# Kernel optimization log

Hardware: AMD Instinct MI355X
Metric: run time of the kernel (lower is better)

Reference implementation:

```python
import jax, jax.numpy as jnp
import numpy as np

D_PAIR = 128
N_HEAD = 4
D_HID = 32
SCALING = 1.0 / np.sqrt(D_HID)


def setup_inputs() -> dict:
    key = jax.random.key(0)
    ks = jax.random.split(key, 12)
    B, L = 1, 256
    s = 0.02
    return {
        "pair": jax.random.normal(ks[0], (B, L, L, D_PAIR), dtype=jnp.float32),
        "gamma": jnp.ones((D_PAIR,), jnp.float32),
        "beta": jnp.zeros((D_PAIR,), jnp.float32),
        "Wq": jax.random.normal(ks[1], (D_PAIR, N_HEAD * D_HID), jnp.float32) * s,
        "Wk": jax.random.normal(ks[2], (D_PAIR, N_HEAD * D_HID), jnp.float32) * s,
        "Wv": jax.random.normal(ks[3], (D_PAIR, N_HEAD * D_HID), jnp.float32) * s,
        "Wb": jax.random.normal(ks[4], (D_PAIR, N_HEAD), jnp.float32) * s,
        "Wg": jax.random.normal(ks[5], (D_PAIR, N_HEAD * D_HID), jnp.float32) * s,
        "bg": jnp.ones((N_HEAD * D_HID,), jnp.float32),
        "Wo": jax.random.normal(ks[6], (N_HEAD * D_HID, D_PAIR), jnp.float32) * s,
        "bo": jnp.zeros((D_PAIR,), jnp.float32),
    }


def _layernorm(x, gamma, beta, eps=1e-5):
    mu = jnp.mean(x, axis=-1, keepdims=True)
    var = jnp.var(x, axis=-1, keepdims=True)
    return (x - mu) * jax.lax.rsqrt(var + eps) * gamma + beta


def reference(pair, gamma, beta, Wq, Wk, Wv, Wb, Wg, bg, Wo, bo):
    B, L = pair.shape[:2]
    x = _layernorm(pair, gamma, beta)                      # (B,L,L,D)
    q = (x @ Wq).reshape(B, L, L, N_HEAD, D_HID) * SCALING  # (B,L,L,h,d)
    k = (x @ Wk).reshape(B, L, L, N_HEAD, D_HID)
    v = (x @ Wv).reshape(B, L, L, N_HEAD, D_HID)
    bias = x @ Wb                                           # (B,L,L,h)
    gate = jax.nn.sigmoid(x @ Wg + bg)                      # (B,L,L,h*d)
    # start_node=True: attend over ending index k of row i
    attn = jnp.einsum('bijhd,bikhd->bijkh', q, k)           # (B,L,L,L,h)
    attn = attn + bias[:, None]                             # bias[b,j,k,h] broadcast over i
    attn = jax.nn.softmax(attn, axis=-2)                    # over k
    out = jnp.einsum('bijkh,bikhd->bijhd', attn, v).reshape(B, L, L, N_HEAD * D_HID)
    out = gate * out
    return out @ Wo + bo
```

## Files before the change

kernel.cpp:

```cpp
#include <hip/hip_runtime.h>
#include <math.h>

#define L 256
#define DP 128
#define NH 4
#define DH 32
#define NROW 65536

typedef unsigned short ushort_t;
typedef __attribute__((ext_vector_type(8))) short short8;
typedef __attribute__((ext_vector_type(4))) float f32x4;
typedef __attribute__((ext_vector_type(4))) unsigned int u32x4;

constexpr float SCALING = 0.17677669529663687f;

static __device__ __forceinline__ unsigned short f2bf(float f) {
    unsigned u = __builtin_bit_cast(unsigned, f);
    u = u + 0x7fffu + ((u >> 16) & 1u);
    return (unsigned short)(u >> 16);
}
static __device__ __forceinline__ float bf2f(unsigned short h) {
    unsigned u = ((unsigned)h) << 16;
    return __builtin_bit_cast(float, u);
}
static __device__ __forceinline__ unsigned packbf(float lo, float hi) {
    return ((unsigned)f2bf(hi) << 16) | (unsigned)f2bf(lo);
}

__global__ __launch_bounds__(256) void prep_kernel(
    const float* __restrict__ Wq, const float* __restrict__ Wk, const float* __restrict__ Wv,
    const float* __restrict__ Wb, const float* __restrict__ Wg, const float* __restrict__ Wo,
    ushort_t* __restrict__ WtAll, ushort_t* __restrict__ WohT, ushort_t* __restrict__ WolT)
{
    int rowi = blockIdx.x * 16 + (threadIdx.x >> 4);
    int d0 = (threadIdx.x & 15) * 8;
    #pragma unroll
    for (int dd = 0; dd < 8; ++dd) {
        int d = d0 + dd;
        if (rowi < 512) {
            int n = rowi & 127;
            float val;
            if (rowi < 128)      val = Wq[d * 128 + n] * SCALING;
            else if (rowi < 256) val = Wk[d * 128 + n];
            else if (rowi < 384) val = Wv[d * 128 + n];
            else                 val = Wg[d * 128 + n];
            WtAll[rowi * 128 + d] = f2bf(val);
        } else if (rowi < 516) {
            WtAll[rowi * 128 + d] = f2bf(Wb[d * 4 + (rowi - 512)]);
        } else if (rowi < 528) {
            WtAll[rowi * 128 + d] = 0;
        } else if (rowi < 656) {
            int n = rowi - 528;
            WohT[n * 128 + d] = f2bf(Wo[d * 128 + n]);
        } else {
            int n = rowi - 656;
            float wv = Wo[d * 128 + n];
            unsigned short hb = f2bf(wv);
            WolT[n * 128 + d] = f2bf(wv - bf2f(hb));
        }
    }
}

__global__ __launch_bounds__(256) void ln_proj_mfma(
    const float* __restrict__ pair, const float* __restrict__ gamma, const float* __restrict__ beta,
    const ushort_t* __restrict__ WtAll, const float* __restrict__ bgv,
    ushort_t* __restrict__ qo, ushort_t* __restrict__ ko, ushort_t* __restrict__ vo,
    float* __restrict__ gateo, float* __restrict__ biasT)
{
    __shared__ __align__(16) unsigned char xs[64 * 256];

    const int t = threadIdx.x;
    const int w = t >> 6, lane = t & 63;
    const int c = lane & 15, g = lane >> 4;
    const int base = blockIdx.x * 64;

    {
        const float* pr = pair + ((size_t)base + w * 16) * DP;
        float e0[16], e1[16];
        #pragma unroll
        for (int r = 0; r < 16; ++r) {
            e0[r] = pr[r * DP + lane];
            e1[r] = pr[r * DP + 64 + lane];
        }
        const float g0 = gamma[lane], g1 = gamma[lane + 64];
        const float b0 = beta[lane],  b1 = beta[lane + 64];
        #pragma unroll
        for (int r = 0; r < 16; ++r) {
            float s = e0[r] + e1[r], ss = e0[r] * e0[r] + e1[r] * e1[r];
            #pragma unroll
            for (int o = 32; o > 0; o >>= 1) { s += __shfl_xor(s, o); ss += __shfl_xor(ss, o); }
            float mu = s * (1.f / DP);
            float rq = rsqrtf(ss * (1.f / DP) - mu * mu + 1e-5f);
            int rl = w * 16 + r;
            unsigned swz = (unsigned)((rl & 7) << 4);
            *(ushort_t*)(xs + (((unsigned)(rl * 256 + 2 * lane)) ^ swz)) = f2bf((e0[r] - mu) * rq * g0 + b0);
            *(ushort_t*)(xs + (((unsigned)(rl * 256 + 2 * (lane + 64))) ^ swz)) = f2bf((e1[r] - mu) * rq * g1 + b1);
        }
    }
    __syncthreads();

    const int mtot = (w == 3) ? 9 : 8;
    for (int m = 0; m < mtot; ++m) {
        const int nt = (m < 8) ? (w + 4 * m) : 32;
        const ushort_t* wbp = WtAll + (size_t)(nt * 16 + c) * 128 + 8 * g;
        short8 bw[4];
        #pragma unroll
        for (int kk = 0; kk < 4; ++kk) bw[kk] = *(const short8*)(wbp + kk * 32);

        const int n = nt * 16 + c;
        #pragma unroll
        for (int rg = 0; rg < 4; ++rg) {
            const int rl = rg * 16 + c;
            const unsigned swz = (unsigned)((rl & 7) << 4);
            f32x4 acc = {0.f, 0.f, 0.f, 0.f};
            #pragma unroll
            for (int kk = 0; kk < 4; ++kk) {
                short8 af = *(const short8*)(xs + (((unsigned)(rl * 256 + kk * 64 + g * 16)) ^ swz));
                acc = __builtin_amdgcn_mfma_f32_16x16x32_bf16(af, bw[kk], acc, 0, 0, 0);
            }
            const int rowb = base + rg * 16 + 4 * g;
            if (nt < 8) {
                #pragma unroll
                for (int e = 0; e < 4; ++e) qo[(size_t)(rowb + e) * 128 + n] = f2bf(acc[e]);
            } else if (nt < 16) {
                #pragma unroll
                for (int e = 0; e < 4; ++e) ko[(size_t)(rowb + e) * 128 + (n - 128)] = f2bf(acc[e]);
            } else if (nt < 24) {
                #pragma unroll
                for (int e = 0; e < 4; ++e) vo[(size_t)(rowb + e) * 128 + (n - 256)] = f2bf(acc[e]);
            } else if (nt < 32) {
                float bgn = bgv[n - 384];
                #pragma unroll
                for (int e = 0; e < 4; ++e)
                    gateo[(size_t)(rowb + e) * 128 + (n - 384)] = 1.f / (1.f + __expf(-(acc[e] + bgn)));
            } else {
                if (c < 4) {
                    #pragma unroll
                    for (int e = 0; e < 4; ++e)
                        biasT[(size_t)c * NROW + rowb + e] = acc[e];
                }
            }
        }
    }
}

__global__ __launch_bounds__(256) void attn_mfma(
    const ushort_t* __restrict__ qbf, const ushort_t* __restrict__ kbf, const ushort_t* __restrict__ vbf,
    const float* __restrict__ biasT, float* __restrict__ ao)
{
    __shared__ __align__(16) unsigned char Kb[256 * 64];
    __shared__ __align__(16) unsigned char Vt[32 * 512];

    const int h = blockIdx.x & 3, i = blockIdx.x >> 2;
    const int t = threadIdx.x, w = t >> 6, lane = t & 63;
    const int c = lane & 15, g = lane >> 4;

    {
        const ushort_t* kg = kbf + (size_t)(i * 256) * 128 + h * 32;
        #pragma unroll
        for (int it = 0; it < 8; ++it) {
            int idx = it * 256 + t;
            int kr = idx >> 3, dp = idx & 7;
            *(uint2*)(Kb + kr * 64 + dp * 8) = *(const uint2*)(kg + (size_t)kr * 128 + dp * 4);
        }
    }
    {
        const ushort_t* vg = vbf + (size_t)(i * 256) * 128 + h * 32;
        #pragma unroll
        for (int it = 0; it < 4; ++it) {
            int idx = it * 256 + t;
            int kp = idx >> 3, dp = idx & 7;
            int kt = kp >> 4, cc = kp & 15;
            int a = cc & 3, gg = cc >> 2;
            int k1 = (a < 2) ? (4 * gg + 2 * a) : (12 + 4 * gg + 2 * a);
            int r0 = kt * 32 + k1;
            uint2 va = *(const uint2*)(vg + (size_t)r0 * 128 + dp * 4);
            uint2 vb = *(const uint2*)(vg + (size_t)(r0 + 1) * 128 + dp * 4);
            unsigned av[4] = { va.x & 0xffffu, va.x >> 16, va.y & 0xffffu, va.y >> 16 };
            unsigned bv[4] = { vb.x & 0xffffu, vb.x >> 16, vb.y & 0xffffu, vb.y >> 16 };
            int kcolb = kt * 64 + 4 * cc;
            #pragma unroll
            for (int dd = 0; dd < 4; ++dd) {
                int d = 4 * dp + dd;
                unsigned pk = (bv[dd] << 16) | av[dd];
                *(unsigned*)(Vt + (((unsigned)(d * 512 + kcolb)) ^ ((unsigned)((d & 7) << 4)))) = pk;
            }
        }
    }
    __syncthreads();

    const int j0 = w * 64;
    short8 qf[4];
    {
        const ushort_t* qg = qbf + (size_t)(i * 256 + j0) * 128 + h * 32;
        #pragma unroll
        for (int jt = 0; jt < 4; ++jt)
            qf[jt] = *(const short8*)(qg + (size_t)(jt * 16 + c) * 128 + 8 * g);
    }

    const float* biasH = biasT + (size_t)h * NROW;

    f32x4 O[4][2];
    float rsum[4] = {0.f, 0.f, 0.f, 0.f};
    #pragma unroll
    for (int jt = 0; jt < 4; ++jt) {
        O[jt][0] = (f32x4){0.f, 0.f, 0.f, 0.f};
        O[jt][1] = (f32x4){0.f, 0.f, 0.f, 0.f};
    }

    for (int kt = 0; kt < 8; ++kt) {
        short8 kf[2];
        #pragma unroll
        for (int ks = 0; ks < 2; ++ks)
            kf[ks] = *(const short8*)(Kb + (kt * 32 + ks * 16 + c) * 64 + g * 16);
        short8 vb0 = *(const short8*)(Vt + (((unsigned)(c * 512 + kt * 64 + g * 16)) ^ ((unsigned)((c & 7) << 4))));
        short8 vb1 = *(const short8*)(Vt + (((unsigned)((16 + c) * 512 + kt * 64 + g * 16)) ^ ((unsigned)(((16 + c) & 7) << 4))));

        #pragma unroll
        for (int jt = 0; jt < 4; ++jt) {
            f32x4 s0, s1;
            {
                f32x4 z = {0.f, 0.f, 0.f, 0.f};
                s0 = __builtin_amdgcn_mfma_f32_16x16x32_bf16(kf[0], qf[jt], z, 0, 0, 0);
                s1 = __builtin_amdgcn_mfma_f32_16x16x32_bf16(kf[1], qf[jt], z, 0, 0, 0);
            }
            const int jrow = j0 + jt * 16 + c;
            const f32x4 b0 = *(const f32x4*)(biasH + (size_t)jrow * 256 + kt * 32 + 4 * g);
            const f32x4 b1 = *(const f32x4*)(biasH + (size_t)jrow * 256 + kt * 32 + 16 + 4 * g);
            #pragma unroll
            for (int e = 0; e < 4; ++e) {
                s0[e] = __expf(s0[e] + b0[e]);
                s1[e] = __expf(s1[e] + b1[e]);
            }
            rsum[jt] += (s0[0] + s0[1] + s0[2] + s0[3]) + (s1[0] + s1[1] + s1[2] + s1[3]);
            u32x4 pk;
            pk[0] = packbf(s0[0], s0[1]);
            pk[1] = packbf(s0[2], s0[3]);
            pk[2] = packbf(s1[0], s1[1]);
            pk[3] = packbf(s1[2], s1[3]);
            short8 pa = __builtin_bit_cast(short8, pk);
            O[jt][0] = __builtin_amdgcn_mfma_f32_16x16x32_bf16(vb0, pa, O[jt][0], 0, 0, 0);
            O[jt][1] = __builtin_amdgcn_mfma_f32_16x16x32_bf16(vb1, pa, O[jt][1], 0, 0, 0);
        }
    }

    #pragma unroll
    for (int jt = 0; jt < 4; ++jt) {
        float v = rsum[jt];
        v += __shfl_xor(v, 16);
        v += __shfl_xor(v, 32);
        rsum[jt] = 1.f / v;
    }
    float* aoB = ao + (size_t)(i * 256 + j0) * 128 + h * 32;
    #pragma unroll
    for (int jt = 0; jt < 4; ++jt) {
        const float inv = rsum[jt];
        #pragma unroll
        for (int dt = 0; dt < 2; ++dt) {
            f32x4 ov;
            #pragma unroll
            for (int e = 0; e < 4; ++e) ov[e] = O[jt][dt][e] * inv;
            *(f32x4*)(aoB + (size_t)(jt * 16 + c) * 128 + dt * 16 + 4 * g) = ov;
        }
    }
}

__global__ __launch_bounds__(256) void out_proj_mfma(
    const float* __restrict__ gate, const float* __restrict__ ao,
    const ushort_t* __restrict__ WohT, const ushort_t* __restrict__ WolT,
    const float* __restrict__ bo, float* __restrict__ out)
{
    const int t = threadIdx.x;
    const int w = t >> 6, lane = t & 63;
    const int c = lane & 15, g = lane >> 4;
    const int base = blockIdx.x * 64;

    const size_t arow = (size_t)(base + w * 16 + c) * 128;
    short8 ah[4], al[4];
    #pragma unroll
    for (int kk = 0; kk < 4; ++kk) {
        const float* gp = gate + arow + kk * 32 + g * 8;
        const float* ap = ao + arow + kk * 32 + g * 8;
        f32x4 g0 = *(const f32x4*)gp, g1 = *(const f32x4*)(gp + 4);
        f32x4 a0 = *(const f32x4*)ap, a1 = *(const f32x4*)(ap + 4);
        short8 hv, lv;
        #pragma unroll
        for (int e = 0; e < 4; ++e) {
            float x0 = g0[e] * a0[e];
            float x1 = g1[e] * a1[e];
            unsigned short h0 = f2bf(x0), h1 = f2bf(x1);
            hv[e] = (short)h0; hv[e + 4] = (short)h1;
            lv[e] = (short)f2bf(x0 - bf2f(h0)); lv[e + 4] = (short)f2bf(x1 - bf2f(h1));
        }
        ah[kk] = hv; al[kk] = lv;
    }

    const int rowb = base + w * 16 + 4 * g;
    #pragma unroll 2
    for (int nt = 0; nt < 8; ++nt) {
        f32x4 acc = {0.f, 0.f, 0.f, 0.f};
        const ushort_t* wh = WohT + (size_t)(nt * 16 + c) * 128 + 8 * g;
        const ushort_t* wl = WolT + (size_t)(nt * 16 + c) * 128 + 8 * g;
        #pragma unroll
        for (int kk = 0; kk < 4; ++kk) {
            short8 bh = *(const short8*)(wh + kk * 32);
            short8 bl = *(const short8*)(wl + kk * 32);
            acc = __builtin_amdgcn_mfma_f32_16x16x32_bf16(ah[kk], bh, acc, 0, 0, 0);
            acc = __builtin_amdgcn_mfma_f32_16x16x32_bf16(ah[kk], bl, acc, 0, 0, 0);
            acc = __builtin_amdgcn_mfma_f32_16x16x32_bf16(al[kk], bh, acc, 0, 0, 0);
        }
        int n = nt * 16 + c;
        float bon = bo[n];
        #pragma unroll
        for (int e = 0; e < 4; ++e)
            out[(size_t)(rowb + e) * 128 + n] = acc[e] + bon;
    }
}

extern "C" void kernel_launch(void* const* d_in, const int* in_sizes, int n_in,
                              void* d_out, int out_size, void* d_ws, size_t ws_size,
                              hipStream_t stream) {
    const float* pair  = (const float*)d_in[0];
    const float* gamma = (const float*)d_in[1];
    const float* beta  = (const float*)d_in[2];
    const float* Wq    = (const float*)d_in[3];
    const float* Wk    = (const float*)d_in[4];
    const float* Wv    = (const float*)d_in[5];
    const float* Wb    = (const float*)d_in[6];
    const float* Wg    = (const float*)d_in[7];
    const float* bg    = (const float*)d_in[8];
    const float* Wo    = (const float*)d_in[9];
    const float* bo    = (const float*)d_in[10];

    unsigned char* ws = (unsigned char*)d_ws;
    size_t off = 0;
    ushort_t* q_bf   = (ushort_t*)(ws + off); off += (size_t)NROW * 128 * 2;
    ushort_t* k_bf   = (ushort_t*)(ws + off); off += (size_t)NROW * 128 * 2;
    ushort_t* v_bf   = (ushort_t*)(ws + off); off += (size_t)NROW * 128 * 2;
    float*    gateo  = (float*)(ws + off);    off += (size_t)NROW * 128 * 4;
    float*    ao     = (float*)(ws + off);    off += (size_t)NROW * 128 * 4;
    float*    biasT  = (float*)(ws + off);    off += (size_t)NH * NROW * 4;
    ushort_t* WtAll  = (ushort_t*)(ws + off); off += 528 * 128 * 2;
    ushort_t* WohT   = (ushort_t*)(ws + off); off += 128 * 128 * 2;
    ushort_t* WolT   = (ushort_t*)(ws + off); off += 128 * 128 * 2;

    prep_kernel<<<49, 256, 0, stream>>>(Wq, Wk, Wv, Wb, Wg, Wo, WtAll, WohT, WolT);
    ln_proj_mfma<<<NROW / 64, 256, 0, stream>>>(pair, gamma, beta, WtAll, bg,
                                                q_bf, k_bf, v_bf, gateo, biasT);
    attn_mfma<<<L * NH, 256, 0, stream>>>(q_bf, k_bf, v_bf, biasT, ao);
    out_proj_mfma<<<NROW / 64, 256, 0, stream>>>(gateo, ao, WohT, WolT, bo, (float*)d_out);
}
```

Baseline: 232.4 us.

## Fuse gating into attention epilogue, store gate as bf16, hoist LDS A-fragments

The sigmoid gate is now stored as bf16 instead of fp32. The attention kernel applies the gate and the hi/lo bf16 split in its epilogue and writes two bf16 arrays. The output projection then loads these pre-split operands directly instead of reading fp32 gate and attention outputs. The projection kernel also loads all LayerNorm A-fragments from LDS into registers once, instead of reloading them for every N tile. This cuts global memory traffic between kernels and repeated LDS reads, at the cost of gate precision and extra register pressure.

```diff
diff --git a/kernel.cpp b/kernel.cpp
--- a/kernel.cpp
+++ b/kernel.cpp
@@ -65,7 +65,7 @@
     const float* __restrict__ pair, const float* __restrict__ gamma, const float* __restrict__ beta,
     const ushort_t* __restrict__ WtAll, const float* __restrict__ bgv,
     ushort_t* __restrict__ qo, ushort_t* __restrict__ ko, ushort_t* __restrict__ vo,
-    float* __restrict__ gateo, float* __restrict__ biasT)
+    ushort_t* __restrict__ gateo, float* __restrict__ biasT)
 {
     __shared__ __align__(16) unsigned char xs[64 * 256];
 
@@ -99,6 +99,16 @@
     }
     __syncthreads();
 
+    short8 af[4][4];
+    #pragma unroll
+    for (int rg = 0; rg < 4; ++rg) {
+        const int rl = rg * 16 + c;
+        const unsigned swz = (unsigned)((rl & 7) << 4);
+        #pragma unroll
+        for (int kk = 0; kk < 4; ++kk)
+            af[rg][kk] = *(const short8*)(xs + (((unsigned)(rl * 256 + kk * 64 + g * 16)) ^ swz));
+    }
+
     const int mtot = (w == 3) ? 9 : 8;
     for (int m = 0; m < mtot; ++m) {
         const int nt = (m < 8) ? (w + 4 * m) : 32;
@@ -110,14 +120,11 @@
         const int n = nt * 16 + c;
         #pragma unroll
         for (int rg = 0; rg < 4; ++rg) {
-            const int rl = rg * 16 + c;
-            const unsigned swz = (unsigned)((rl & 7) << 4);
             f32x4 acc = {0.f, 0.f, 0.f, 0.f};
             #pragma unroll
-            for (int kk = 0; kk < 4; ++kk) {
-                short8 af = *(const short8*)(xs + (((unsigned)(rl * 256 + kk * 64 + g * 16)) ^ swz));
-                acc = __builtin_amdgcn_mfma_f32_16x16x32_bf16(af, bw[kk], acc, 0, 0, 0);
-            }
+            for (int kk = 0; kk < 4; ++kk)
+                acc = __builtin_amdgcn_mfma_f32_16x16x32_bf16(af[rg][kk], bw[kk], acc, 0, 0, 0);
+
             const int rowb = base + rg * 16 + 4 * g;
             if (nt < 8) {
                 #pragma unroll
@@ -132,7 +139,8 @@
                 float bgn = bgv[n - 384];
                 #pragma unroll
                 for (int e = 0; e < 4; ++e)
-                    gateo[(size_t)(rowb + e) * 128 + (n - 384)] = 1.f / (1.f + __expf(-(acc[e] + bgn)));
+                    gateo[(size_t)(rowb + e) * 128 + (n - 384)] =
+                        f2bf(1.f / (1.f + __expf(-(acc[e] + bgn))));
             } else {
                 if (c < 4) {
                     #pragma unroll
@@ -146,7 +154,8 @@
 
 __global__ __launch_bounds__(256) void attn_mfma(
     const ushort_t* __restrict__ qbf, const ushort_t* __restrict__ kbf, const ushort_t* __restrict__ vbf,
-    const float* __restrict__ biasT, float* __restrict__ ao)
+    const ushort_t* __restrict__ gbf, const float* __restrict__ biasT,
+    ushort_t* __restrict__ xh, ushort_t* __restrict__ xl)
 {
     __shared__ __align__(16) unsigned char Kb[256 * 64];
     __shared__ __align__(16) unsigned char Vt[32 * 512];
@@ -251,22 +260,37 @@
         v += __shfl_xor(v, 32);
         rsum[jt] = 1.f / v;
     }
-    float* aoB = ao + (size_t)(i * 256 + j0) * 128 + h * 32;
+    const ushort_t* gB = gbf + (size_t)(i * 256 + j0) * 128 + h * 32;
+    ushort_t* xhB = xh + (size_t)(i * 256 + j0) * 128 + h * 32;
+    ushort_t* xlB = xl + (size_t)(i * 256 + j0) * 128 + h * 32;
     #pragma unroll
     for (int jt = 0; jt < 4; ++jt) {
         const float inv = rsum[jt];
         #pragma unroll
         for (int dt = 0; dt < 2; ++dt) {
-            f32x4 ov;
-            #pragma unroll
-            for (int e = 0; e < 4; ++e) ov[e] = O[jt][dt][e] * inv;
-            *(f32x4*)(aoB + (size_t)(jt * 16 + c) * 128 + dt * 16 + 4 * g) = ov;
+            const int off = (jt * 16 + c) * 128 + dt * 16 + 4 * g;
+            uint2 gv = *(const uint2*)(gB + off);
+            unsigned gs[4] = { gv.x & 0xffffu, gv.x >> 16, gv.y & 0xffffu, gv.y >> 16 };
+            float xq[4];
+            unsigned short hq[4];
+            #pragma unroll
+            for (int e = 0; e < 4; ++e) {
+                xq[e] = bf2f((unsigned short)gs[e]) * O[jt][dt][e] * inv;
+                hq[e] = f2bf(xq[e]);
+            }
+            uint2 hv, lv;
+            hv.x = ((unsigned)hq[1] << 16) | hq[0];
+            hv.y = ((unsigned)hq[3] << 16) | hq[2];
+            lv.x = packbf(xq[0] - bf2f(hq[0]), xq[1] - bf2f(hq[1]));
+            lv.y = packbf(xq[2] - bf2f(hq[2]), xq[3] - bf2f(hq[3]));
+            *(uint2*)(xhB + off) = hv;
+            *(uint2*)(xlB + off) = lv;
         }
     }
 }
 
 __global__ __launch_bounds__(256) void out_proj_mfma(
-    const float* __restrict__ gate, const float* __restrict__ ao,
+    const ushort_t* __restrict__ xh, const ushort_t* __restrict__ xl,
     const ushort_t* __restrict__ WohT, const ushort_t* __restrict__ WolT,
     const float* __restrict__ bo, float* __restrict__ out)
 {
@@ -279,20 +303,8 @@
     short8 ah[4], al[4];
     #pragma unroll
     for (int kk = 0; kk < 4; ++kk) {
-        const float* gp = gate + arow + kk * 32 + g * 8;
-        const float* ap = ao + arow + kk * 32 + g * 8;
-        f32x4 g0 = *(const f32x4*)gp, g1 = *(const f32x4*)(gp + 4);
-        f32x4 a0 = *(const f32x4*)ap, a1 = *(const f32x4*)(ap + 4);
-        short8 hv, lv;
-        #pragma unroll
-        for (int e = 0; e < 4; ++e) {
-            float x0 = g0[e] * a0[e];
-            float x1 = g1[e] * a1[e];
-            unsigned short h0 = f2bf(x0), h1 = f2bf(x1);
-            hv[e] = (short)h0; hv[e + 4] = (short)h1;
-            lv[e] = (short)f2bf(x0 - bf2f(h0)); lv[e + 4] = (short)f2bf(x1 - bf2f(h1));
-        }
-        ah[kk] = hv; al[kk] = lv;
+        ah[kk] = *(const short8*)(xh + arow + kk * 32 + g * 8);
+        al[kk] = *(const short8*)(xl + arow + kk * 32 + g * 8);
     }
 
     const int rowb = base + w * 16 + 4 * g;
@@ -337,8 +349,9 @@
     ushort_t* q_bf   = (ushort_t*)(ws + off); off += (size_t)NROW * 128 * 2;
     ushort_t* k_bf   = (ushort_t*)(ws + off); off += (size_t)NROW * 128 * 2;
     ushort_t* v_bf   = (ushort_t*)(ws + off); off += (size_t)NROW * 128 * 2;
-    float*    gateo  = (float*)(ws + off);    off += (size_t)NROW * 128 * 4;
-    float*    ao     = (float*)(ws + off);    off += (size_t)NROW * 128 * 4;
+    ushort_t* g_bf   = (ushort_t*)(ws + off); off += (size_t)NROW * 128 * 2;
+    ushort_t* xh_bf  = (ushort_t*)(ws + off); off += (size_t)NROW * 128 * 2;
+    ushort_t* xl_bf  = (ushort_t*)(ws + off); off += (size_t)NROW * 128 * 2;
     float*    biasT  = (float*)(ws + off);    off += (size_t)NH * NROW * 4;
     ushort_t* WtAll  = (ushort_t*)(ws + off); off += 528 * 128 * 2;
     ushort_t* WohT   = (ushort_t*)(ws + off); off += 128 * 128 * 2;
@@ -346,7 +359,7 @@
 
     prep_kernel<<<49, 256, 0, stream>>>(Wq, Wk, Wv, Wb, Wg, Wo, WtAll, WohT, WolT);
     ln_proj_mfma<<<NROW / 64, 256, 0, stream>>>(pair, gamma, beta, WtAll, bg,
-                                                q_bf, k_bf, v_bf, gateo, biasT);
-    attn_mfma<<<L * NH, 256, 0, stream>>>(q_bf, k_bf, v_bf, biasT, ao);
-    out_proj_mfma<<<NROW / 64, 256, 0, stream>>>(gateo, ao, WohT, WolT, bo, (float*)d_out);
-}
+                                                q_bf, k_bf, v_bf, g_bf, biasT);
+    attn_mfma<<<L * NH, 256, 0, stream>>>(q_bf, k_bf, v_bf, g_bf, biasT, xh_bf, xl_bf);
+    out_proj_mfma<<<NROW / 64, 256, 0, stream>>>(xh_bf, xl_bf, WohT, WolT, bo, (float*)d_out);
+}
```

Result: no change. 232.0 us (-0.1%).
